# Performance work log

Measured on AMD Instinct MI355X. Metric: run time of the kernel, lower is better.

The kernel has to match this reference:

```python
import jax, jax.numpy as jnp
import numpy as np

N_EMBD = 768
N_HEAD = 12


def setup_inputs() -> dict:
    key = jax.random.key(0)
    k1, k2, k3, k4, k5 = jax.random.split(key, 5)
    B, T, C = 2, 2048, N_EMBD
    s = 1.0 / np.sqrt(C)
    x = jax.random.normal(k1, (B, T, C), dtype=jnp.float32)
    W_attn = jax.random.uniform(k2, (C, 3 * C), dtype=jnp.float32, minval=-s, maxval=s)
    b_attn = jax.random.uniform(k3, (3 * C,), dtype=jnp.float32, minval=-s, maxval=s)
    W_proj = jax.random.uniform(k4, (C, C), dtype=jnp.float32, minval=-s, maxval=s)
    b_proj = jax.random.uniform(k5, (C,), dtype=jnp.float32, minval=-s, maxval=s)
    return {"x": x, "W_attn": W_attn, "b_attn": b_attn, "W_proj": W_proj, "b_proj": b_proj}


def reference(x, W_attn, b_attn, W_proj, b_proj):
    B, T, C = x.shape
    H = N_HEAD
    D = C // H
    qkv = x @ W_attn + b_attn                      # [B,T,3C]
    q, k, v = jnp.split(qkv, 3, axis=-1)
    q = q.reshape(B, T, H, D).transpose(0, 2, 1, 3)  # [B,H,T,D]
    k = k.reshape(B, T, H, D).transpose(0, 2, 1, 3)
    v = v.reshape(B, T, H, D).transpose(0, 2, 1, 3)
    scale = 1.0 / jnp.sqrt(jnp.asarray(D, dtype=x.dtype))
    scores = jnp.einsum("bhqd,bhkd->bhqk", q, k) * scale  # [B,H,T,T]
    causal = jnp.tril(jnp.ones((T, T), dtype=bool))
    scores = jnp.where(causal, scores, jnp.finfo(x.dtype).min)
    attn = jax.nn.softmax(scores, axis=-1)
    y = jnp.einsum("bhqk,bhkd->bhqd", attn, v)     # [B,H,T,D]
    y = y.transpose(0, 2, 1, 3).reshape(B, T, C)
    return y @ W_proj + b_proj
```

## Files before the change

kernel.cpp:

```cpp
#include <hip/hip_runtime.h>
#include <math.h>

#define N_EMBD 768
#define N_HEAD 12
#define HEAD_DIM 64
#define SEQ 2048
#define BATCH 2

typedef __attribute__((ext_vector_type(8))) short v8s;
typedef __attribute__((ext_vector_type(4))) float v4f;

__device__ __forceinline__ unsigned short f2bf(float f) {
    union { float f; unsigned int u; } x; x.f = f;
    unsigned int u = x.u + 0x7fffu + ((x.u >> 16) & 1u);
    return (unsigned short)(u >> 16);
}
__device__ __forceinline__ float bf2f(unsigned short s) {
    union { unsigned int u; float f; } x; x.u = ((unsigned int)s) << 16;
    return x.f;
}
__device__ __forceinline__ unsigned int pack_bf16(float lo, float hi) {
    unsigned int ul = __float_as_uint(lo) + 0x8000u;
    unsigned int uh = __float_as_uint(hi) + 0x8000u;
    return __builtin_amdgcn_perm(uh, ul, 0x07060302);
}

__device__ __forceinline__ void gload_lds16(const unsigned short* g, unsigned short* l) {
    __builtin_amdgcn_global_load_lds(
        (const __attribute__((address_space(1))) void*)g,
        (__attribute__((address_space(3))) void*)l, 16, 0, 0);
}

#define QSCALE 0.1803368801111396f

__global__ __launch_bounds__(256) void prep_kernel(
    const float* __restrict__ x,
    const float* __restrict__ W_attn,
    const float* __restrict__ W_proj,
    unsigned short* __restrict__ xb,
    unsigned short* __restrict__ wta,
    unsigned short* __restrict__ wtp)
{
    __shared__ float t[32][33];
    const int blk = (int)blockIdx.x;
    if (blk < 1536) {
        const int i = (blk * 256 + threadIdx.x) * 8;
        const float4 a = *(const float4*)(x + i);
        const float4 b = *(const float4*)(x + i + 4);
        ushort4 s0, s1;
        s0.x = f2bf(a.x); s0.y = f2bf(a.y); s0.z = f2bf(a.z); s0.w = f2bf(a.w);
        s1.x = f2bf(b.x); s1.y = f2bf(b.y); s1.z = f2bf(b.z); s1.w = f2bf(b.w);
        *(ushort4*)(xb + i) = s0;
        *(ushort4*)(xb + i + 4) = s1;
        return;
    }
    const float* in; unsigned short* out; int R, C, bx, by;
    if (blk < 1536 + 1728) {
        const int b2 = blk - 1536;
        in = W_attn; out = wta; R = 768; C = 2304;
        bx = (b2 % 72) * 32; by = (b2 / 72) * 32;
    } else {
        const int b2 = blk - 3264;
        in = W_proj; out = wtp; R = 768; C = 768;
        bx = (b2 % 24) * 32; by = (b2 / 24) * 32;
    }
    const int tx = threadIdx.x & 31, ty = threadIdx.x >> 5;
#pragma unroll
    for (int i = 0; i < 32; i += 8)
        t[ty + i][tx] = in[(size_t)(by + ty + i) * C + bx + tx];
    __syncthreads();
#pragma unroll
    for (int i = 0; i < 32; i += 8)
        out[(size_t)(bx + ty + i) * R + by + tx] = f2bf(t[tx][ty + i]);
}

__global__ __launch_bounds__(256) void qkv_gemm_mfma(
    const unsigned short* __restrict__ A,
    const unsigned short* __restrict__ Bt,
    const float* __restrict__ bias,
    unsigned short* __restrict__ qg,
    unsigned short* __restrict__ kg,
    unsigned short* __restrict__ vg)
{
    __shared__ unsigned short as[2][128 * 32];
    __shared__ unsigned short bs[2][64 * 32];
    const int K = 768;
    const int tid = threadIdx.x;
    const int lane = tid & 63;
    const int w = tid >> 6;
    const int wm = w >> 1, wn = w & 1;
    const int quad = lane >> 4, c = lane & 15;
    const int bm = blockIdx.y * 128;
    const int bn = blockIdx.x * 64;

    const int srow = tid >> 2;
    const int soff = (tid & 3) * 8;
    const unsigned short* ap  = A  + (size_t)(bm + srow) * K + soff;
    const unsigned short* ap2 = A  + (size_t)(bm + 64 + srow) * K + soff;
    const unsigned short* bp  = Bt + (size_t)(bn + srow) * K + soff;

    v4f acc[4][2];
#pragma unroll
    for (int i = 0; i < 4; i++)
#pragma unroll
        for (int j = 0; j < 2; j++) acc[i][j] = (v4f){0.f, 0.f, 0.f, 0.f};

    gload_lds16(ap,  &as[0][tid * 8]);
    gload_lds16(ap2, &as[0][(256 + tid) * 8]);
    gload_lds16(bp,  &bs[0][tid * 8]);

    int bufi = 0;
    for (int k0 = 0; k0 < K; k0 += 32, bufi ^= 1) {
        __syncthreads();
        if (k0 + 32 < K) {
            const int kn = k0 + 32;
            gload_lds16(ap + kn,  &as[bufi ^ 1][tid * 8]);
            gload_lds16(ap2 + kn, &as[bufi ^ 1][(256 + tid) * 8]);
            gload_lds16(bp + kn,  &bs[bufi ^ 1][tid * 8]);
        }

        v8s af[4], bf[2];
#pragma unroll
        for (int fm = 0; fm < 4; fm++)
            af[fm] = *(const v8s*)&as[bufi][(wm * 64 + fm * 16 + c) * 32 + quad * 8];
#pragma unroll
        for (int fn = 0; fn < 2; fn++)
            bf[fn] = *(const v8s*)&bs[bufi][(wn * 32 + fn * 16 + c) * 32 + quad * 8];
#pragma unroll
        for (int fm = 0; fm < 4; fm++)
#pragma unroll
            for (int fn = 0; fn < 2; fn++)
                acc[fm][fn] = __builtin_amdgcn_mfma_f32_16x16x32_bf16(af[fm], bf[fn], acc[fm][fn], 0, 0, 0);
    }

    const int which = bn / N_EMBD;
    const int h = (bn - which * N_EMBD) >> 6;
#pragma unroll
    for (int fm = 0; fm < 4; fm++) {
        const int m0 = bm + wm * 64 + fm * 16 + quad * 4;
        const int b = m0 >> 11;
        const int t0 = m0 & (SEQ - 1);
        const size_t bh = (size_t)(b * N_HEAD + h);
#pragma unroll
        for (int fn = 0; fn < 2; fn++) {
            const int d = wn * 32 + fn * 16 + c;
            const float bv = bias[bn + d];
            if (which == 2) {
                ushort4 o;
                o.x = f2bf(acc[fm][fn][0] + bv);
                o.y = f2bf(acc[fm][fn][1] + bv);
                o.z = f2bf(acc[fm][fn][2] + bv);
                o.w = f2bf(acc[fm][fn][3] + bv);
                *(ushort4*)(vg + (bh * 64 + d) * SEQ + t0) = o;
            } else {
                unsigned short* dst = (which == 0) ? qg : kg;
                const float sc = (which == 0) ? QSCALE : 1.0f;
#pragma unroll
                for (int r = 0; r < 4; r++)
                    dst[(bh * SEQ + t0 + r) * 64 + d] = f2bf((acc[fm][fn][r] + bv) * sc);
            }
        }
    }
}

__global__ __launch_bounds__(256) void attn_kernel(
    const unsigned short* __restrict__ qg,
    const unsigned short* __restrict__ kg,
    const unsigned short* __restrict__ vg,
    unsigned short* __restrict__ pO,
    float* __restrict__ pl,
    unsigned short* __restrict__ y)
{
    __shared__ __align__(16) unsigned short ks[2][64 * 64];
    __shared__ __align__(16) unsigned short vs[2][64 * 64];
    __shared__ __align__(16) unsigned short ps[4][16 * 64];

    const int tid  = threadIdx.x;
    const int w    = tid >> 6;
    const int lane = tid & 63;
    const int quad = lane >> 4;
    const int c    = lane & 15;

    const int bid = (int)blockIdx.x;
    const int bh  = bid % 24;
    const int c2  = 79 - (bid / 24);
    int qt, kc;
    if (c2 < 8)       { qt = c2;                    kc = 0; }
    else if (c2 < 24) { qt = 8 + ((c2 - 8) >> 1);   kc = (c2 - 8) & 1; }
    else if (c2 < 48) { qt = 16 + (c2 - 24) / 3;    kc = (c2 - 24) % 3; }
    else              { qt = 24 + ((c2 - 48) >> 2); kc = (c2 - 48) & 3; }
    const int qbase = qt * 64;

    const unsigned short* qrow = qg + (size_t)bh * SEQ * 64;
    const unsigned short* krow = kg + (size_t)bh * SEQ * 64;
    const unsigned short* vrow = vg + (size_t)bh * 64 * SEQ;

    const unsigned short* qp = qrow + (size_t)(qbase + w * 16 + c) * 64 + quad * 8;
    const v8s bq0 = *(const v8s*)(qp);
    const v8s bq1 = *(const v8s*)(qp + 32);

    const int r0 = tid >> 3;
    const int ch0 = (tid & 7) ^ (r0 & 7);
    const unsigned short* kp0 = krow + (size_t)r0 * 64 + ch0 * 8;
    const unsigned short* vp0 = vrow + (size_t)r0 * SEQ + ch0 * 8;

    const int swz0 = ((quad ^ (c & 7)) * 8);
    const int swz1 = swz0 ^ 32;

    v4f oacc[4];
#pragma unroll
    for (int d = 0; d < 4; d++) oacc[d] = (v4f){0.f, 0.f, 0.f, 0.f};
    float l_acc = 0.f;

    const int q_lane = qbase + w * 16 + c;
    unsigned int* pw32 = (unsigned int*)&ps[w][0];
    const int psq = c & 7;

    const int kt0 = kc * 8;
    const int kt1 = min(kt0 + 8, qt + 1);

    {
        const int key0 = kt0 * 64;
        const int b = kt0 & 1;
        gload_lds16(kp0 + (size_t)key0 * 64, &ks[b][tid * 8]);
        gload_lds16(kp0 + (size_t)(key0 + 32) * 64, &ks[b][(256 + tid) * 8]);
        gload_lds16(vp0 + key0, &vs[b][tid * 8]);
        gload_lds16(vp0 + 32 * SEQ + key0, &vs[b][(256 + tid) * 8]);
    }

    for (int kt = kt0; kt < kt1; kt++) {
        const int b = kt & 1;
        __syncthreads();
        if (kt + 1 < kt1) {
            const int key0n = (kt + 1) * 64;
            gload_lds16(kp0 + (size_t)key0n * 64, &ks[b ^ 1][tid * 8]);
            gload_lds16(kp0 + (size_t)(key0n + 32) * 64, &ks[b ^ 1][(256 + tid) * 8]);
            gload_lds16(vp0 + key0n, &vs[b ^ 1][tid * 8]);
            gload_lds16(vp0 + 32 * SEQ + key0n, &vs[b ^ 1][(256 + tid) * 8]);
        }
        const int key0 = kt * 64;

        v4f sacc[4];
#pragma unroll
        for (int n = 0; n < 4; n++) {
            const int rb = (n * 16 + c) * 64;
            const v8s ak0 = *(const v8s*)&ks[b][rb + swz0];
            const v8s ak1 = *(const v8s*)&ks[b][rb + swz1];
            v4f s = (v4f){0.f, 0.f, 0.f, 0.f};
            s = __builtin_amdgcn_mfma_f32_16x16x32_bf16(ak0, bq0, s, 0, 0, 0);
            s = __builtin_amdgcn_mfma_f32_16x16x32_bf16(ak1, bq1, s, 0, 0, 0);
            sacc[n] = s;
        }

        if (kt == qt) {
            const int kb = key0 + quad * 4;
#pragma unroll
            for (int n = 0; n < 4; n++)
#pragma unroll
                for (int r = 0; r < 4; r++)
                    if (kb + n * 16 + r > q_lane) sacc[n][r] = -1e30f;
        }

#pragma unroll
        for (int n = 0; n < 4; n++) {
            const float p0 = exp2f(sacc[n][0]);
            const float p1 = exp2f(sacc[n][1]);
            const float p2 = exp2f(sacc[n][2]);
            const float p3 = exp2f(sacc[n][3]);
            l_acc += (p0 + p1) + (p2 + p3);
            const int sswz = (2 * n + (quad >> 1)) ^ psq;
            const int dw = c * 32 + sswz * 4 + (quad & 1) * 2;
            pw32[dw]     = pack_bf16(p0, p1);
            pw32[dw + 1] = pack_bf16(p2, p3);
        }

        const v8s ap0 = *(const v8s*)&ps[w][c * 64 + swz0];
        const v8s ap1 = *(const v8s*)&ps[w][c * 64 + swz1];
#pragma unroll
        for (int d = 0; d < 4; d++) {
            const int rb = (d * 16 + c) * 64;
            const v8s bv0 = *(const v8s*)&vs[b][rb + swz0];
            const v8s bv1 = *(const v8s*)&vs[b][rb + swz1];
            oacc[d] = __builtin_amdgcn_mfma_f32_16x16x32_bf16(ap0, bv0, oacc[d], 0, 0, 0);
            oacc[d] = __builtin_amdgcn_mfma_f32_16x16x32_bf16(ap1, bv1, oacc[d], 0, 0, 0);
        }
    }

    l_acc += __shfl_xor(l_acc, 16, 64);
    l_acc += __shfl_xor(l_acc, 32, 64);

    if (c2 < 8) {
        const int b = bh / N_HEAD;
        const int h = bh - b * N_HEAD;
#pragma unroll
        for (int r = 0; r < 4; r++) {
            const float inv = 1.0f / __shfl(l_acc, quad * 4 + r, 64);
            const int tq = qbase + w * 16 + quad * 4 + r;
            unsigned short* yr = y + ((size_t)(b * SEQ + tq)) * N_EMBD + h * 64;
#pragma unroll
            for (int d = 0; d < 4; d++)
                yr[d * 16 + c] = f2bf(oacc[d][r] * inv);
        }
        return;
    }

    const size_t pidx = (size_t)bh * 80 + c2;
    unsigned short* po = pO + pidx * 4096;
#pragma unroll
    for (int r = 0; r < 4; r++) {
        const int row = w * 16 + quad * 4 + r;
#pragma unroll
        for (int d = 0; d < 4; d++)
            po[row * 64 + d * 16 + c] = f2bf(oacc[d][r]);
    }
    if (lane < 16)
        pl[pidx * 64 + w * 16 + c] = l_acc;
}

__global__ __launch_bounds__(256) void combine_kernel(
    const unsigned short* __restrict__ pO,
    const float* __restrict__ pl,
    unsigned short* __restrict__ y)
{
    const int qt = 8 + (int)blockIdx.x;
    const int bh = (int)blockIdx.y;
    int base, nc;
    if (qt < 16)      { base = 8 + 2 * (qt - 8);   nc = 2; }
    else if (qt < 24) { base = 24 + 3 * (qt - 16); nc = 3; }
    else              { base = 48 + 4 * (qt - 24); nc = 4; }

    const int row = threadIdx.x >> 2;
    const int colg = (threadIdx.x & 3) * 16;

    float denom = 0.f;
    for (int i = 0; i < nc; i++)
        denom += pl[((size_t)bh * 80 + base + i) * 64 + row];
    const float inv = 1.0f / denom;

    float acc[16];
#pragma unroll
    for (int j = 0; j < 16; j++) acc[j] = 0.f;
    for (int i = 0; i < nc; i++) {
        const unsigned short* po = pO + ((size_t)bh * 80 + base + i) * 4096 + row * 64 + colg;
        ushort4 u0 = *(const ushort4*)(po + 0);
        ushort4 u1 = *(const ushort4*)(po + 4);
        ushort4 u2 = *(const ushort4*)(po + 8);
        ushort4 u3 = *(const ushort4*)(po + 12);
        acc[0]  += bf2f(u0.x); acc[1]  += bf2f(u0.y);
        acc[2]  += bf2f(u0.z); acc[3]  += bf2f(u0.w);
        acc[4]  += bf2f(u1.x); acc[5]  += bf2f(u1.y);
        acc[6]  += bf2f(u1.z); acc[7]  += bf2f(u1.w);
        acc[8]  += bf2f(u2.x); acc[9]  += bf2f(u2.y);
        acc[10] += bf2f(u2.z); acc[11] += bf2f(u2.w);
        acc[12] += bf2f(u3.x); acc[13] += bf2f(u3.y);
        acc[14] += bf2f(u3.z); acc[15] += bf2f(u3.w);
    }

    const int b = bh / N_HEAD;
    const int h = bh - b * N_HEAD;
    const int t = qt * 64 + row;
    unsigned short* yr = y + ((size_t)(b * SEQ + t)) * N_EMBD + h * 64 + colg;
    ushort4 o0, o1, o2, o3;
    o0.x = f2bf(acc[0] * inv);  o0.y = f2bf(acc[1] * inv);
    o0.z = f2bf(acc[2] * inv);  o0.w = f2bf(acc[3] * inv);
    o1.x = f2bf(acc[4] * inv);  o1.y = f2bf(acc[5] * inv);
    o1.z = f2bf(acc[6] * inv);  o1.w = f2bf(acc[7] * inv);
    o2.x = f2bf(acc[8] * inv);  o2.y = f2bf(acc[9] * inv);
    o2.z = f2bf(acc[10] * inv); o2.w = f2bf(acc[11] * inv);
    o3.x = f2bf(acc[12] * inv); o3.y = f2bf(acc[13] * inv);
    o3.z = f2bf(acc[14] * inv); o3.w = f2bf(acc[15] * inv);
    *(ushort4*)(yr + 0)  = o0;
    *(ushort4*)(yr + 4)  = o1;
    *(ushort4*)(yr + 8)  = o2;
    *(ushort4*)(yr + 12) = o3;
}

__global__ __launch_bounds__(256) void proj_gemm_mfma(
    const unsigned short* __restrict__ A,
    const unsigned short* __restrict__ Bt,
    const float* __restrict__ bias,
    float* __restrict__ out)
{
    __shared__ unsigned short as[2][128 * 32];
    __shared__ unsigned short bs[2][128 * 32];
    const int K = 768;
    const int tid = threadIdx.x;
    const int lane = tid & 63;
    const int w = tid >> 6;
    const int wm = w >> 1, wn = w & 1;
    const int quad = lane >> 4, c = lane & 15;
    const int bm = blockIdx.y * 128;
    const int bn = blockIdx.x * 128;

    const int srow = tid >> 2;
    const int soff = (tid & 3) * 8;
    const unsigned short* ap = A  + (size_t)(bm + srow) * K + soff;
    const unsigned short* bp = Bt + (size_t)(bn + srow) * K + soff;
    const unsigned short* ap2 = A  + (size_t)(bm + 64 + srow) * K + soff;
    const unsigned short* bp2 = Bt + (size_t)(bn + 64 + srow) * K + soff;

    v4f acc[4][4];
#pragma unroll
    for (int i = 0; i < 4; i++)
#pragma unroll
        for (int j = 0; j < 4; j++) acc[i][j] = (v4f){0.f, 0.f, 0.f, 0.f};

    gload_lds16(ap, &as[0][tid * 8]);
    gload_lds16(ap2, &as[0][(256 + tid) * 8]);
    gload_lds16(bp, &bs[0][tid * 8]);
    gload_lds16(bp2, &bs[0][(256 + tid) * 8]);

    int bufi = 0;
    for (int k0 = 0; k0 < K; k0 += 32, bufi ^= 1) {
        __syncthreads();
        if (k0 + 32 < K) {
            const int kn = k0 + 32;
            gload_lds16(ap + kn, &as[bufi ^ 1][tid * 8]);
            gload_lds16(ap2 + kn, &as[bufi ^ 1][(256 + tid) * 8]);
            gload_lds16(bp + kn, &bs[bufi ^ 1][tid * 8]);
            gload_lds16(bp2 + kn, &bs[bufi ^ 1][(256 + tid) * 8]);
        }

        v8s af[4], bf[4];
#pragma unroll
        for (int fm = 0; fm < 4; fm++)
            af[fm] = *(const v8s*)&as[bufi][(wm * 64 + fm * 16 + c) * 32 + quad * 8];
#pragma unroll
        for (int fn = 0; fn < 4; fn++)
            bf[fn] = *(const v8s*)&bs[bufi][(wn * 64 + fn * 16 + c) * 32 + quad * 8];
#pragma unroll
        for (int fm = 0; fm < 4; fm++)
#pragma unroll
            for (int fn = 0; fn < 4; fn++)
                acc[fm][fn] = __builtin_amdgcn_mfma_f32_16x16x32_bf16(af[fm], bf[fn], acc[fm][fn], 0, 0, 0);
    }

#pragma unroll
    for (int fm = 0; fm < 4; fm++) {
        const int m0 = bm + wm * 64 + fm * 16 + quad * 4;
#pragma unroll
        for (int fn = 0; fn < 4; fn++) {
            const int n = bn + wn * 64 + fn * 16 + c;
            const float bv = bias[n];
#pragma unroll
            for (int r = 0; r < 4; r++)
                out[(size_t)(m0 + r) * N_EMBD + n] = acc[fm][fn][r] + bv;
        }
    }
}

extern "C" void kernel_launch(void* const* d_in, const int* in_sizes, int n_in,
                              void* d_out, int out_size, void* d_ws, size_t ws_size,
                              hipStream_t stream) {
    const float* x      = (const float*)d_in[0];
    const float* W_attn = (const float*)d_in[1];
    const float* b_attn = (const float*)d_in[2];
    const float* W_proj = (const float*)d_in[3];
    const float* b_proj = (const float*)d_in[4];
    float* out = (float*)d_out;

    const size_t QSZ = (size_t)BATCH * N_HEAD * SEQ * HEAD_DIM;

    unsigned short* base = (unsigned short*)d_ws;
    unsigned short* xb  = base;
    unsigned short* wta = base + QSZ;
    unsigned short* pO  = base;
    float* pl = (float*)(base + (size_t)1920 * 4096);
    unsigned short* wtp = (unsigned short*)(pl + 1920 * 64);
    unsigned short* qg  = wtp + (size_t)N_EMBD * N_EMBD;
    unsigned short* kg  = qg + QSZ;
    unsigned short* vg  = kg + QSZ;
    unsigned short* yb  = vg + QSZ;

    prep_kernel<<<dim3(3840), 256, 0, stream>>>(x, W_attn, W_proj, xb, wta, wtp);
    qkv_gemm_mfma<<<dim3(36, 32), 256, 0, stream>>>(xb, wta, b_attn, qg, kg, vg);
    attn_kernel<<<dim3(80 * 24), 256, 0, stream>>>(qg, kg, vg, pO, pl, yb);
    combine_kernel<<<dim3(24, BATCH * N_HEAD), 256, 0, stream>>>(pO, pl, yb);
    proj_gemm_mfma<<<dim3(6, 32), 256, 0, stream>>>(yb, wtp, b_proj, out);
}
```

Baseline: 162.3 us.

## Enlarge QKV GEMM tiles with swizzled LDS and shrink projection GEMM tiles

The QKV GEMM moves from 128x64 tiles with K-step 32 to 128x128 tiles with K-step 64. Its shared-memory layout gets an XOR swizzle to avoid bank conflicts, which cuts global traffic and barriers per MFMA. The projection GEMM goes the other way, from 128x128 to 64x64 tiles, so it launches 768 blocks instead of 192 and fills more CUs. The tradeoff is higher LDS use (64KB) and more registers in the QKV kernel, which can lower occupancy, and less operand reuse in the projection.

```diff
diff --git a/kernel.cpp b/kernel.cpp
--- a/kernel.cpp
+++ b/kernel.cpp
@@ -82,8 +82,8 @@
     unsigned short* __restrict__ kg,
     unsigned short* __restrict__ vg)
 {
-    __shared__ unsigned short as[2][128 * 32];
-    __shared__ unsigned short bs[2][64 * 32];
+    __shared__ __align__(16) unsigned short as[2][128 * 64];
+    __shared__ __align__(16) unsigned short bs[2][128 * 64];
     const int K = 768;
     const int tid = threadIdx.x;
     const int lane = tid & 63;
@@ -91,60 +91,73 @@
     const int wm = w >> 1, wn = w & 1;
     const int quad = lane >> 4, c = lane & 15;
     const int bm = blockIdx.y * 128;
-    const int bn = blockIdx.x * 64;
-
-    const int srow = tid >> 2;
-    const int soff = (tid & 3) * 8;
-    const unsigned short* ap  = A  + (size_t)(bm + srow) * K + soff;
-    const unsigned short* ap2 = A  + (size_t)(bm + 64 + srow) * K + soff;
-    const unsigned short* bp  = Bt + (size_t)(bn + srow) * K + soff;
-
-    v4f acc[4][2];
+    const int bn = blockIdx.x * 128;
+
+    const int r0 = tid >> 3;
+    const int kosw = ((tid & 7) ^ (r0 & 7)) * 8;
+    const unsigned short* ap = A  + (size_t)(bm + r0) * K + kosw;
+    const unsigned short* bp = Bt + (size_t)(bn + r0) * K + kosw;
+
+    v4f acc[4][4];
 #pragma unroll
     for (int i = 0; i < 4; i++)
 #pragma unroll
-        for (int j = 0; j < 2; j++) acc[i][j] = (v4f){0.f, 0.f, 0.f, 0.f};
-
-    gload_lds16(ap,  &as[0][tid * 8]);
-    gload_lds16(ap2, &as[0][(256 + tid) * 8]);
-    gload_lds16(bp,  &bs[0][tid * 8]);
+        for (int j = 0; j < 4; j++) acc[i][j] = (v4f){0.f, 0.f, 0.f, 0.f};
+
+#pragma unroll
+    for (int p = 0; p < 4; p++) {
+        gload_lds16(ap + (size_t)p * 32 * K, &as[0][(tid + p * 256) * 8]);
+        gload_lds16(bp + (size_t)p * 32 * K, &bs[0][(tid + p * 256) * 8]);
+    }
 
     int bufi = 0;
-    for (int k0 = 0; k0 < K; k0 += 32, bufi ^= 1) {
+    for (int k0 = 0; k0 < K; k0 += 64, bufi ^= 1) {
         __syncthreads();
-        if (k0 + 32 < K) {
-            const int kn = k0 + 32;
-            gload_lds16(ap + kn,  &as[bufi ^ 1][tid * 8]);
-            gload_lds16(ap2 + kn, &as[bufi ^ 1][(256 + tid) * 8]);
-            gload_lds16(bp + kn,  &bs[bufi ^ 1][tid * 8]);
-        }
-
-        v8s af[4], bf[2];
-#pragma unroll
-        for (int fm = 0; fm < 4; fm++)
-            af[fm] = *(const v8s*)&as[bufi][(wm * 64 + fm * 16 + c) * 32 + quad * 8];
-#pragma unroll
-        for (int fn = 0; fn < 2; fn++)
-            bf[fn] = *(const v8s*)&bs[bufi][(wn * 32 + fn * 16 + c) * 32 + quad * 8];
-#pragma unroll
-        for (int fm = 0; fm < 4; fm++)
-#pragma unroll
-            for (int fn = 0; fn < 2; fn++)
-                acc[fm][fn] = __builtin_amdgcn_mfma_f32_16x16x32_bf16(af[fm], bf[fn], acc[fm][fn], 0, 0, 0);
+        if (k0 + 64 < K) {
+            const int kn = k0 + 64;
+#pragma unroll
+            for (int p = 0; p < 4; p++) {
+                gload_lds16(ap + kn + (size_t)p * 32 * K, &as[bufi ^ 1][(tid + p * 256) * 8]);
+                gload_lds16(bp + kn + (size_t)p * 32 * K, &bs[bufi ^ 1][(tid + p * 256) * 8]);
+            }
+        }
+
+#pragma unroll
+        for (int kh = 0; kh < 2; kh++) {
+            v8s af[4], bf[4];
+#pragma unroll
+            for (int fm = 0; fm < 4; fm++) {
+                const int row = wm * 64 + fm * 16 + c;
+                const int swz = ((kh * 4 + quad) ^ (c & 7)) * 8;
+                af[fm] = *(const v8s*)&as[bufi][row * 64 + swz];
+            }
+#pragma unroll
+            for (int fn = 0; fn < 4; fn++) {
+                const int row = wn * 64 + fn * 16 + c;
+                const int swz = ((kh * 4 + quad) ^ (c & 7)) * 8;
+                bf[fn] = *(const v8s*)&bs[bufi][row * 64 + swz];
+            }
+#pragma unroll
+            for (int fm = 0; fm < 4; fm++)
+#pragma unroll
+                for (int fn = 0; fn < 4; fn++)
+                    acc[fm][fn] = __builtin_amdgcn_mfma_f32_16x16x32_bf16(af[fm], bf[fn], acc[fm][fn], 0, 0, 0);
+        }
     }
 
     const int which = bn / N_EMBD;
-    const int h = (bn - which * N_EMBD) >> 6;
+    const int rem_base = bn - which * N_EMBD;
 #pragma unroll
     for (int fm = 0; fm < 4; fm++) {
         const int m0 = bm + wm * 64 + fm * 16 + quad * 4;
         const int b = m0 >> 11;
         const int t0 = m0 & (SEQ - 1);
-        const size_t bh = (size_t)(b * N_HEAD + h);
-#pragma unroll
-        for (int fn = 0; fn < 2; fn++) {
-            const int d = wn * 32 + fn * 16 + c;
-            const float bv = bias[bn + d];
+#pragma unroll
+        for (int fn = 0; fn < 4; fn++) {
+            const int rem = rem_base + wn * 64 + fn * 16 + c;
+            const int h = rem >> 6, d = rem & 63;
+            const float bv = bias[bn + wn * 64 + fn * 16 + c];
+            const size_t bh = (size_t)(b * N_HEAD + h);
             if (which == 2) {
                 ushort4 o;
                 o.x = f2bf(acc[fm][fn][0] + bv);
@@ -381,34 +394,30 @@
     const float* __restrict__ bias,
     float* __restrict__ out)
 {
-    __shared__ unsigned short as[2][128 * 32];
-    __shared__ unsigned short bs[2][128 * 32];
+    __shared__ unsigned short as[2][64 * 32];
+    __shared__ unsigned short bs[2][64 * 32];
     const int K = 768;
     const int tid = threadIdx.x;
     const int lane = tid & 63;
     const int w = tid >> 6;
     const int wm = w >> 1, wn = w & 1;
     const int quad = lane >> 4, c = lane & 15;
-    const int bm = blockIdx.y * 128;
-    const int bn = blockIdx.x * 128;
+    const int bm = blockIdx.y * 64;
+    const int bn = blockIdx.x * 64;
 
     const int srow = tid >> 2;
     const int soff = (tid & 3) * 8;
     const unsigned short* ap = A  + (size_t)(bm + srow) * K + soff;
     const unsigned short* bp = Bt + (size_t)(bn + srow) * K + soff;
-    const unsigned short* ap2 = A  + (size_t)(bm + 64 + srow) * K + soff;
-    const unsigned short* bp2 = Bt + (size_t)(bn + 64 + srow) * K + soff;
-
-    v4f acc[4][4];
-#pragma unroll
-    for (int i = 0; i < 4; i++)
-#pragma unroll
-        for (int j = 0; j < 4; j++) acc[i][j] = (v4f){0.f, 0.f, 0.f, 0.f};
+
+    v4f acc[2][2];
+#pragma unroll
+    for (int i = 0; i < 2; i++)
+#pragma unroll
+        for (int j = 0; j < 2; j++) acc[i][j] = (v4f){0.f, 0.f, 0.f, 0.f};
 
     gload_lds16(ap, &as[0][tid * 8]);
-    gload_lds16(ap2, &as[0][(256 + tid) * 8]);
     gload_lds16(bp, &bs[0][tid * 8]);
-    gload_lds16(bp2, &bs[0][(256 + tid) * 8]);
 
     int bufi = 0;
     for (int k0 = 0; k0 < K; k0 += 32, bufi ^= 1) {
@@ -416,31 +425,29 @@
         if (k0 + 32 < K) {
             const int kn = k0 + 32;
             gload_lds16(ap + kn, &as[bufi ^ 1][tid * 8]);
-            gload_lds16(ap2 + kn, &as[bufi ^ 1][(256 + tid) * 8]);
             gload_lds16(bp + kn, &bs[bufi ^ 1][tid * 8]);
-            gload_lds16(bp2 + kn, &bs[bufi ^ 1][(256 + tid) * 8]);
-        }
-
-        v8s af[4], bf[4];
-#pragma unroll
-        for (int fm = 0; fm < 4; fm++)
-            af[fm] = *(const v8s*)&as[bufi][(wm * 64 + fm * 16 + c) * 32 + quad * 8];
-#pragma unroll
-        for (int fn = 0; fn < 4; fn++)
-            bf[fn] = *(const v8s*)&bs[bufi][(wn * 64 + fn * 16 + c) * 32 + quad * 8];
-#pragma unroll
-        for (int fm = 0; fm < 4; fm++)
-#pragma unroll
-            for (int fn = 0; fn < 4; fn++)
+        }
+
+        v8s af[2], bf[2];
+#pragma unroll
+        for (int fm = 0; fm < 2; fm++)
+            af[fm] = *(const v8s*)&as[bufi][(wm * 32 + fm * 16 + c) * 32 + quad * 8];
+#pragma unroll
+        for (int fn = 0; fn < 2; fn++)
+            bf[fn] = *(const v8s*)&bs[bufi][(wn * 32 + fn * 16 + c) * 32 + quad * 8];
+#pragma unroll
+        for (int fm = 0; fm < 2; fm++)
+#pragma unroll
+            for (int fn = 0; fn < 2; fn++)
                 acc[fm][fn] = __builtin_amdgcn_mfma_f32_16x16x32_bf16(af[fm], bf[fn], acc[fm][fn], 0, 0, 0);
     }
 
 #pragma unroll
-    for (int fm = 0; fm < 4; fm++) {
-        const int m0 = bm + wm * 64 + fm * 16 + quad * 4;
-#pragma unroll
-        for (int fn = 0; fn < 4; fn++) {
-            const int n = bn + wn * 64 + fn * 16 + c;
+    for (int fm = 0; fm < 2; fm++) {
+        const int m0 = bm + wm * 32 + fm * 16 + quad * 4;
+#pragma unroll
+        for (int fn = 0; fn < 2; fn++) {
+            const int n = bn + wn * 32 + fn * 16 + c;
             const float bv = bias[n];
 #pragma unroll
             for (int r = 0; r < 4; r++)
@@ -473,8 +480,8 @@
     unsigned short* yb  = vg + QSZ;
 
     prep_kernel<<<dim3(3840), 256, 0, stream>>>(x, W_attn, W_proj, xb, wta, wtp);
-    qkv_gemm_mfma<<<dim3(36, 32), 256, 0, stream>>>(xb, wta, b_attn, qg, kg, vg);
+    qkv_gemm_mfma<<<dim3(18, 32), 256, 0, stream>>>(xb, wta, b_attn, qg, kg, vg);
     attn_kernel<<<dim3(80 * 24), 256, 0, stream>>>(qg, kg, vg, pO, pl, yb);
     combine_kernel<<<dim3(24, BATCH * N_HEAD), 256, 0, stream>>>(pO, pl, yb);
-    proj_gemm_mfma<<<dim3(6, 32), 256, 0, stream>>>(yb, wtp, b_proj, out);
-}
+    proj_gemm_mfma<<<dim3(12, 64), 256, 0, stream>>>(yb, wtp, b_proj, out);
+}
```

Measured after the change: 167.6 us. +3.3%, slower.
